# Kernel optimization log

Measured on AMD Instinct MI355X. Metric: run time of the kernel, lower is better.

## Reference

```python
import jax, jax.numpy as jnp
import numpy as np

EPS = 1e-5
NEG = 0.1  # LeakyReLU slope


def _conv(x, w, stride=1, pad=0):
    return jax.lax.conv_general_dilated(
        x, w, (stride, stride), [(pad, pad), (pad, pad)],
        dimension_numbers=('NCHW', 'OIHW', 'NCHW'))


def _bn(x, p):
    # p: [4, C] stacked (gamma, beta, running_mean, running_var); eval-mode BN
    g, b, m, v = p[0], p[1], p[2], p[3]
    inv = g / jnp.sqrt(v + EPS)
    return x * inv[None, :, None, None] + (b - m * inv)[None, :, None, None]


def _lrelu(x):
    return jnp.where(x >= 0, x, NEG * x)


def _mdcn(x, w_off, b_off, w_dcn, b_dcn, G=2, K=3, pad=1):
    # ModulatedDeformConvPack (DCNv2): conv_offset -> (dy, dx, mask), then
    # modulated bilinear sampling + dense contraction with the conv weight.
    B, C, H, W = x.shape
    K2 = K * K
    off = _conv(x, w_off, 1, pad) + b_off[None, :, None, None]  # [B, 3*G*K2, H, W]
    dy, dx, ml = jnp.split(off, 3, axis=1)
    dy = dy.reshape(B, G, K2, H, W)
    dx = dx.reshape(B, G, K2, H, W)
    mask = jax.nn.sigmoid(ml).reshape(B, G, K2, H, W)
    kyv, kxv = np.meshgrid(np.arange(K), np.arange(K), indexing='ij')
    ky = jnp.asarray(kyv.reshape(K2), x.dtype)
    kx = jnp.asarray(kxv.reshape(K2), x.dtype)
    ii = jnp.arange(H, dtype=x.dtype)
    jj = jnp.arange(W, dtype=x.dtype)
    # sample coords: p0 + p_k + offset (stride 1, dilation 1)
    py = ii[None, None, None, :, None] - pad + ky[None, None, :, None, None] + dy
    px = jj[None, None, None, None, :] - pad + kx[None, None, :, None, None] + dx
    Cg = C // G
    # [B, G, H*W, Cg] layout so the bilinear gather indexes a small int tensor
    imgs = x.reshape(B, G, Cg, H, W).transpose(0, 1, 3, 4, 2).reshape(B, G, H * W, Cg)
    y0 = jnp.floor(py)
    x0 = jnp.floor(px)
    N = K2 * H * W
    wy = (py - y0).reshape(B, G, N, 1)
    wx = (px - x0).reshape(B, G, N, 1)

    def gather(yi, xi):
        valid = (yi >= 0) & (yi <= H - 1) & (xi >= 0) & (xi <= W - 1)
        yc = jnp.clip(yi, 0, H - 1).astype(jnp.int32)
        xc = jnp.clip(xi, 0, W - 1).astype(jnp.int32)
        idx = (yc * W + xc).reshape(B, G, N, 1)
        v = jnp.take_along_axis(imgs, idx, axis=2)  # [B, G, N, Cg]
        return v * valid.reshape(B, G, N, 1).astype(x.dtype)

    v00 = gather(y0, x0)
    v01 = gather(y0, x0 + 1)
    v10 = gather(y0 + 1, x0)
    v11 = gather(y0 + 1, x0 + 1)
    val = (v00 * (1 - wy) * (1 - wx) + v01 * (1 - wy) * wx
           + v10 * wy * (1 - wx) + v11 * wy * wx)
    val = (val * mask.reshape(B, G, N, 1)).reshape(B, G, K2, H, W, Cg)
    wr = w_dcn.reshape(w_dcn.shape[0], G, Cg, K2)
    out = jnp.einsum('bgkijc,ogck->boij', val, wr)
    return out + b_dcn[None, :, None, None]


def _forward(x, w_r1, bn_r1, w_r2, bn_r2, w_rs, bn_rs, w_off, b_off,
             w_dcn, b_dcn, bn1, w_c2, bn2, w_ds, bn_ds):
    # ResBlock(in=64, out=128, stride=2): conv3x3/s2-BN-LReLU-conv3x3-BN + 1x1/s2 shortcut
    h = _lrelu(_bn(_conv(x, w_r1, 2, 1), bn_r1))
    h = _bn(_conv(h, w_r2, 1, 1), bn_r2)
    sc = _bn(_conv(x, w_rs, 2, 0), bn_rs)
    h = _lrelu(h + sc)
    # modulated deformable conv 3x3, deformable_groups=2
    h = _lrelu(_bn(_mdcn(h, w_off, b_off, w_dcn, b_dcn), bn1))
    h = _lrelu(_bn(_conv(h, w_c2, 1, 0), bn2))
    # DeconBlock residual (downsample since in!=out, stride!=1)
    res = _bn(_conv(x, w_ds, 2, 0), bn_ds)
    return res + h


def setup_inputs() -> dict:
    key = jax.random.key(0)
    ks = jax.random.split(key, 16)
    f32 = jnp.float32

    def n(k, shape, s):
        return jax.random.normal(k, shape, f32) * s

    def bnp(k, c):
        # gamma, beta, mean, var — var kept >= 0.1 for stability
        return jax.random.uniform(k, (4, c), f32, 0.1, 1.0)

    return {
        'x': n(ks[0], (4, 64, 192, 192), 1.0),
        'w_r1': n(ks[1], (128, 64, 3, 3), 0.04),
        'bn_r1': bnp(ks[2], 128),
        'w_r2': n(ks[3], (128, 128, 3, 3), 0.03),
        'bn_r2': bnp(ks[4], 128),
        'w_rs': n(ks[5], (128, 64, 1, 1), 0.12),
        'bn_rs': bnp(ks[6], 128),
        'w_off': n(ks[7], (54, 128, 3, 3), 0.01),  # small => offsets of a few px
        'b_off': n(ks[8], (54,), 0.1),
        'w_dcn': n(ks[9], (128, 128, 3, 3), 0.03),
        'b_dcn': n(ks[10], (128,), 0.1),
        'bn1': bnp(ks[11], 128),
        'w_c2': n(ks[12], (128, 128, 1, 1), 0.09),
        'bn2': bnp(ks[13], 128),
        'w_ds': n(ks[14], (128, 64, 1, 1), 0.12),
        'bn_ds': bnp(ks[15], 128),
    }


def reference(x, w_r1, bn_r1, w_r2, bn_r2, w_rs, bn_rs, w_off, b_off,
              w_dcn, b_dcn, bn1, w_c2, bn2, w_ds, bn_ds):
    return _forward(x, w_r1, bn_r1, w_r2, bn_r2, w_rs, bn_rs, w_off, b_off,
                    w_dcn, b_dcn, bn1, w_c2, bn2, w_ds, bn_ds)
```

## Files before the change

### kernel.cpp

```cpp
#include <hip/hip_runtime.h>
#include <hip/hip_bf16.h>
#include <cstdint>

#define EPS 1e-5f
#define NEG 0.1f

using bfrag = __attribute__((ext_vector_type(8))) short;
using f32x4 = __attribute__((ext_vector_type(4))) float;
typedef unsigned short ushort_t;

constexpr int B_  = 4,  CIN = 64, H0 = 192, W0 = 192;
constexpr int C_  = 128, H_ = 96, W_ = 96;
constexpr int HW_ = H_ * W_;
constexpr int HW0 = H0 * W0;
constexpr int XS  = 194;
constexpr int TS  = 98;
constexpr int VROW = 392;

__device__ __forceinline__ ushort_t f2bf(float f) {
  unsigned u = __builtin_bit_cast(unsigned, f);
  u += 0x7fffu + ((u >> 16) & 1u);
  return (ushort_t)(u >> 16);
}
__device__ __forceinline__ float loF(unsigned d) {
  return __builtin_bit_cast(float, d << 16);
}
__device__ __forceinline__ float hiF(unsigned d) {
  return __builtin_bit_cast(float, d & 0xFFFF0000u);
}
__device__ __forceinline__ bfrag loadB(const ushort_t* p) {
  return *(const bfrag*)p;
}

#define MFMA4(A0, A1, B0, B1, ACC)                                             \
  ACC[0][0] = __builtin_amdgcn_mfma_f32_16x16x32_bf16(A0, B0, ACC[0][0], 0, 0, 0); \
  ACC[0][1] = __builtin_amdgcn_mfma_f32_16x16x32_bf16(A0, B1, ACC[0][1], 0, 0, 0); \
  ACC[1][0] = __builtin_amdgcn_mfma_f32_16x16x32_bf16(A1, B0, ACC[1][0], 0, 0, 0); \
  ACC[1][1] = __builtin_amdgcn_mfma_f32_16x16x32_bf16(A1, B1, ACC[1][1], 0, 0, 0);

__global__ __launch_bounds__(256)
void k_prep(const float* __restrict__ x,
            const float* __restrict__ w_r1, const float* __restrict__ w_r2,
            const float* __restrict__ w_off, const float* __restrict__ w_dcn,
            const float* __restrict__ w_rs, const float* __restrict__ w_c2,
            const float* __restrict__ w_ds,
            ushort_t* __restrict__ wp_r1, ushort_t* __restrict__ wp_r2,
            ushort_t* __restrict__ wp_off, ushort_t* __restrict__ wp_dcn,
            ushort_t* __restrict__ wp_rs, ushort_t* __restrict__ wp_c2,
            ushort_t* __restrict__ wp_ds,
            ushort_t* __restrict__ xclp, ushort_t* __restrict__ t1p,
            ushort_t* __restrict__ t3p) {
  __shared__ float tile[64][65];
  int bi = blockIdx.x;
  int tid = (int)threadIdx.x;
  auto pack3w = [&](const float* w, ushort_t* wp, int O, int C, int Opad, int b0) {
    int idx = (bi - b0) * 256 + tid;
    int e = idx & 7;
    int lane = (idx >> 3) & 63;
    int fb = idx >> 9;
    int OBQ = Opad / 16;
    int obq = fb % OBQ, s = fb / OBQ;
    int lr = lane & 15, lq = lane >> 4;
    int o = obq * 16 + lr;
    int cq = s % (C / 32), tap = s / (C / 32);
    int c = cq * 32 + lq * 8 + e;
    wp[idx] = (o < O) ? f2bf(w[((size_t)o * C + c) * 9 + tap]) : (ushort_t)0;
  };
  auto pack1w = [&](const float* w, ushort_t* wp, int O, int C, int Opad, int b0) {
    int idx = (bi - b0) * 256 + tid;
    int e = idx & 7;
    int lane = (idx >> 3) & 63;
    int fb = idx >> 9;
    int OBQ = Opad / 16;
    int obq = fb % OBQ, s = fb / OBQ;
    int lr = lane & 15, lq = lane >> 4;
    int o = obq * 16 + lr;
    int c = s * 32 + lq * 8 + e;
    wp[idx] = (o < O) ? f2bf(w[(size_t)o * C + c]) : (ushort_t)0;
  };
  auto border = [&](ushort_t* buf, int N, int C, int b0) {
    int idx = (bi - b0) * 256 + tid;
    int per = 4 * N - 4;
    if (idx >= per * 4) return;
    int b = idx / per, e = idx - b * per;
    int r, s;
    if (e < N) { r = 0; s = e; }
    else if (e < 2 * N) { r = N - 1; s = e - N; }
    else if (e < 3 * N - 2) { r = e - 2 * N + 1; s = 0; }
    else { r = e - (3 * N - 2) + 1; s = N - 1; }
    uint4* p = (uint4*)(buf + ((size_t)(b * N + r) * N + s) * C);
#pragma unroll
    for (int t = 0; t < 16; ++t) { if (t < C / 8) p[t] = make_uint4(0, 0, 0, 0); }
  };
  if      (bi <  288) pack3w(w_r1,  wp_r1, 128,  64, 128, 0);
  else if (bi <  864) pack3w(w_r2,  wp_r2, 128, 128, 128, 288);
  else if (bi < 1152) pack3w(w_off, wp_off, 54, 128,  64, 864);
  else if (bi < 1728) pack3w(w_dcn, wp_dcn, 128, 128, 128, 1152);
  else if (bi < 1760) pack1w(w_rs,  wp_rs, 128,  64, 128, 1728);
  else if (bi < 1824) pack1w(w_c2,  wp_c2, 128, 128, 128, 1760);
  else if (bi < 1856) pack1w(w_ds,  wp_ds, 128,  64, 128, 1824);
  else if (bi < 1869) border(xclp, XS, 64, 1856);
  else if (bi < 1876) border(t1p, TS, 128, 1869);
  else if (bi < 1883) border(t3p, TS, 128, 1876);
  else {
    int bx = bi - 1883;
    int cx = bx % 3;
    int rem = bx / 3;
    int y = rem % 192, b = rem / 192;
    int tx = tid & 63, ty = tid >> 6;
    const float* src = x + (size_t)b * CIN * HW0 + (size_t)y * W0 + cx * 64;
#pragma unroll
    for (int r = 0; r < 16; ++r) {
      int ch = r * 4 + ty;
      tile[ch][tx] = src[(size_t)ch * HW0 + tx];
    }
    __syncthreads();
    ushort_t* dst = xclp + ((size_t)(b * XS + y + 1) * XS + cx * 64 + 1) * 64;
#pragma unroll
    for (int r = 0; r < 16; ++r) {
      int pp = r * 4 + ty;
      dst[(size_t)pp * 64 + tx] = f2bf(tile[tx][pp]);
    }
  }
}

__global__ __launch_bounds__(256)
void k_conv1(const ushort_t* __restrict__ xclp, const ushort_t* __restrict__ wp,
             const float* __restrict__ bnp, ushort_t* __restrict__ t1p) {
  __shared__ ushort_t at[5 * 66 * 64];
  int tid = threadIdx.x, lane = tid & 63, wv = tid >> 6;
  int lr = lane & 15, lq = lane >> 4, ob = wv * 32;
  int j0 = blockIdx.x * 32, i0 = blockIdx.y * 2, b = blockIdx.z;
  for (int t = tid; t < 2640; t += 256) {
    int ky = t / 528, r = t - ky * 528;
    int p = r >> 3, c8 = r & 7;
    const char* src = (const char*)(xclp +
        ((size_t)(b * XS + 2 * i0 + ky) * XS + 2 * j0) * 64) + p * 128 + c8 * 16;
    int db = ((ky * 66 + p) * 128 + c8 * 16) ^ (((p >> 1) & 7) << 4);
    *(uint4*)((char*)at + db) = *(const uint4*)src;
  }
  __syncthreads();
  f32x4 acc[2][2][2] = {};
#pragma unroll
  for (int tap = 0; tap < 9; ++tap) {
    int ky = tap / 3, kx = tap - 3 * ky;
    int pxa = 2 * lr + kx, pxb = 2 * (16 + lr) + kx;
#pragma unroll
    for (int cq = 0; cq < 2; ++cq) {
      int s = tap * 2 + cq;
      bfrag b0 = loadB(wp + (size_t)(s * 8 + wv * 2) * 512 + lane * 8);
      bfrag b1 = loadB(wp + (size_t)(s * 8 + wv * 2 + 1) * 512 + lane * 8);
#pragma unroll
      for (int r = 0; r < 2; ++r) {
        int kr = 2 * r + ky;
        bfrag a0 = *(const bfrag*)((const char*)at +
            (((kr * 66 + pxa) * 128 + cq * 64 + lq * 16) ^ (((pxa >> 1) & 7) << 4)));
        bfrag a1 = *(const bfrag*)((const char*)at +
            (((kr * 66 + pxb) * 128 + cq * 64 + lq * 16) ^ (((pxb >> 1) & 7) << 4)));
        MFMA4(a0, a1, b0, b1, acc[r]);
      }
    }
  }
#pragma unroll
  for (int r = 0; r < 2; ++r) {
    ushort_t* dst = t1p + ((size_t)(b * TS + i0 + r + 1) * TS + j0 + 1) * 128;
#pragma unroll
    for (int nf = 0; nf < 2; ++nf) {
      int o = ob + nf * 16 + lr;
      float inv = bnp[o] * rsqrtf(bnp[384 + o] + EPS);
      float bb = bnp[128 + o] - bnp[256 + o] * inv;
#pragma unroll
      for (int mf = 0; mf < 2; ++mf)
#pragma unroll
        for (int jj = 0; jj < 4; ++jj) {
          int pix = mf * 16 + 4 * lq + jj;
          float v = acc[r][mf][nf][jj] * inv + bb;
          v = v >= 0.f ? v : NEG * v;
          dst[(size_t)pix * 128 + o] = f2bf(v);
        }
    }
  }
}

__global__ __launch_bounds__(256)
void k_conv2(const ushort_t* __restrict__ t1p, const ushort_t* __restrict__ xclp,
             const ushort_t* __restrict__ wp2, const ushort_t* __restrict__ wprs,
             const float* __restrict__ bn2p, const float* __restrict__ bnsp,
             ushort_t* __restrict__ t3p) {
  __shared__ ushort_t at[4 * 34 * 128];
  int tid = threadIdx.x, lane = tid & 63, wv = tid >> 6;
  int lr = lane & 15, lq = lane >> 4, ob = wv * 32;
  int j0 = blockIdx.x * 32, i0 = blockIdx.y * 2, b = blockIdx.z;
  for (int t = tid; t < 2176; t += 256) {
    int ky = t / 544, r = t - ky * 544;
    int p = r >> 4, c16 = r & 15;
    const char* src = (const char*)(t1p +
        ((size_t)(b * TS + i0 + ky) * TS + j0) * 128) + p * 256 + c16 * 16;
    int db = ((ky * 34 + p) * 256 + c16 * 16) ^ ((p & 7) << 4);
    *(uint4*)((char*)at + db) = *(const uint4*)src;
  }
  __syncthreads();
  f32x4 acc[2][2][2] = {};
  f32x4 acs[2][2][2] = {};
#pragma unroll
  for (int tap = 0; tap < 9; ++tap) {
    int ky = tap / 3, kx = tap - 3 * ky;
    int pxa = lr + kx, pxb = 16 + lr + kx;
#pragma unroll
    for (int cq = 0; cq < 4; ++cq) {
      int s = tap * 4 + cq;
      bfrag b0 = loadB(wp2 + (size_t)(s * 8 + wv * 2) * 512 + lane * 8);
      bfrag b1 = loadB(wp2 + (size_t)(s * 8 + wv * 2 + 1) * 512 + lane * 8);
#pragma unroll
      for (int r = 0; r < 2; ++r) {
        int kr = r + ky;
        bfrag a0 = *(const bfrag*)((const char*)at +
            (((kr * 34 + pxa) * 256 + cq * 64 + lq * 16) ^ ((pxa & 7) << 4)));
        bfrag a1 = *(const bfrag*)((const char*)at +
            (((kr * 34 + pxb) * 256 + cq * 64 + lq * 16) ^ ((pxb & 7) << 4)));
        MFMA4(a0, a1, b0, b1, acc[r]);
      }
    }
  }
#pragma unroll
  for (int r = 0; r < 2; ++r) {
    const ushort_t* rowp = xclp + (size_t)(b * XS + 2 * (i0 + r) + 1) * XS * 64;
    const ushort_t* pa = rowp + (size_t)(2 * (j0 + lr) + 1) * 64 + 8 * lq;
    const ushort_t* pb = rowp + (size_t)(2 * (j0 + 16 + lr) + 1) * 64 + 8 * lq;
#pragma unroll
    for (int sq = 0; sq < 2; ++sq) {
      bfrag a0 = loadB(pa + sq * 32);
      bfrag a1 = loadB(pb + sq * 32);
      bfrag b0 = loadB(wprs + (size_t)(sq * 8 + wv * 2) * 512 + lane * 8);
      bfrag b1 = loadB(wprs + (size_t)(sq * 8 + wv * 2 + 1) * 512 + lane * 8);
      MFMA4(a0, a1, b0, b1, acs[r]);
    }
  }
#pragma unroll
  for (int r = 0; r < 2; ++r) {
    ushort_t* dst = t3p + ((size_t)(b * TS + i0 + r + 1) * TS + j0 + 1) * 128;
#pragma unroll
    for (int nf = 0; nf < 2; ++nf) {
      int o = ob + nf * 16 + lr;
      float i2 = bn2p[o] * rsqrtf(bn2p[384 + o] + EPS);
      float b2 = bn2p[128 + o] - bn2p[256 + o] * i2;
      float is = bnsp[o] * rsqrtf(bnsp[384 + o] + EPS);
      float bs = bnsp[128 + o] - bnsp[256 + o] * is;
#pragma unroll
      for (int mf = 0; mf < 2; ++mf)
#pragma unroll
        for (int jj = 0; jj < 4; ++jj) {
          int pix = mf * 16 + 4 * lq + jj;
          float h = acc[r][mf][nf][jj] * i2 + b2 + acs[r][mf][nf][jj] * is + bs;
          h = h >= 0.f ? h : NEG * h;
          dst[(size_t)pix * 128 + o] = f2bf(h);
        }
    }
  }
}

__global__ __launch_bounds__(512)
void k_dcn(const ushort_t* __restrict__ t3p, const ushort_t* __restrict__ wpo,
           const float* __restrict__ boff, const ushort_t* __restrict__ wp,
           const float* __restrict__ bdcn, const float* __restrict__ bnp,
           ushort_t* __restrict__ t4cl) {
  __shared__ char smem[26112];
  __shared__ float offb_lds[32 * 64];
  int tid = threadIdx.x;
  int j0 = blockIdx.x * 32, i = blockIdx.y, b = blockIdx.z;
  int lane = tid & 63, wv = tid >> 6;
  int lr = lane & 15, lq = lane >> 4;

  {
    for (int t = tid; t < 1632; t += 512) {
      int ky = t / 544, r = t - ky * 544;
      int p = r >> 4, c16b = r & 15;
      const char* src = (const char*)(t3p +
          ((size_t)(b * TS + i + ky) * TS + j0 + p) * 128) + c16b * 16;
      int db = ((ky * 34 + p) * 256 + c16b * 16) ^ ((p & 7) << 4);
      *(uint4*)(smem + db) = *(const uint4*)src;
    }
    __syncthreads();
    int ot = wv >> 1, half = wv & 1;
    f32x4 pacc = {};
#pragma unroll
    for (int s = 0; s < 36; ++s) {
      int tap = s >> 2, cq = s & 3;
      int ky = tap / 3, kx = tap - 3 * ky;
      int px = half * 16 + lr + kx;
      bfrag a0 = *(const bfrag*)(smem +
          (((ky * 34 + px) * 256 + cq * 64 + lq * 16) ^ ((px & 7) << 4)));
      bfrag b0 = loadB(wpo + (size_t)(s * 4 + ot) * 512 + lane * 8);
      pacc = __builtin_amdgcn_mfma_f32_16x16x32_bf16(a0, b0, pacc, 0, 0, 0);
    }
    int o = ot * 16 + lr;
    float bias = (o < 54) ? boff[o] : 0.f;
#pragma unroll
    for (int jj = 0; jj < 4; ++jj) {
      int px = half * 16 + 4 * lq + jj;
      offb_lds[px * 64 + o] = pacc[jj] + bias;
    }
    __syncthreads();
  }

  int gq = tid >> 4;
  int c16 = tid & 15;
  int gl = (gq & 3) * 16;
  int my_b0 = 0, my_b1 = 0;
  unsigned my_w00 = 0, my_w10 = 0, my_w01 = 0, my_w11 = 0;
  if (c16 < 9) {
    int k = c16;
    int ky = k / 3, kx = k - 3 * ky;
    int j = j0 + gq;
    const float* ob_ = offb_lds + gq * 64;
#pragma unroll
    for (int g = 0; g < 2; ++g) {
      int gk = g * 9 + k;
      float dy = ob_[gk];
      float dx = ob_[18 + gk];
      float ml = ob_[36 + gk];
      float mk = 1.f / (1.f + __expf(-ml));
      float py = (float)(i - 1 + ky) + dy;
      float px = (float)(j - 1 + kx) + dx;
      float fy = floorf(py), fx = floorf(px);
      float wy = py - fy, wx = px - fx;
      int y0 = (int)fy, x0 = (int)fx;
      bool yv0 = (unsigned)y0 < 96u, yv1 = (unsigned)(y0 + 1) < 96u;
      bool xv0 = (unsigned)x0 < 96u, xv1 = (unsigned)(x0 + 1) < 96u;
      float w00 = (yv0 && xv0) ? (1.f - wy) * (1.f - wx) * mk : 0.f;
      float w01 = (yv0 && xv1) ? (1.f - wy) * wx * mk : 0.f;
      float w10 = (yv1 && xv0) ? wy * (1.f - wx) * mk : 0.f;
      float w11 = (yv1 && xv1) ? wy * wx * mk : 0.f;
      int yb = min(max(y0, -1), 95), xb = min(max(x0, -1), 95);
      int bb = (((yb + 1) * TS + xb + 1) * 128 + g * 64) * 2;
      unsigned pw0 = (unsigned)f2bf(w00) | ((unsigned)f2bf(w01) << 16);
      unsigned pw1 = (unsigned)f2bf(w10) | ((unsigned)f2bf(w11) << 16);
      if (g == 0) { my_b0 = bb; my_w00 = pw0; my_w10 = pw1; }
      else        { my_b1 = bb; my_w01 = pw0; my_w11 = pw1; }
    }
  }
  __syncthreads();

  ushort_t* val = (ushort_t*)smem;
  const char* imgb = (const char*)(t3p + (size_t)b * TS * TS * 128) + c16 * 8;
  char* vrow = (char*)val + gq * (VROW * 2) + c16 * 8;
  int ob = wv * 16;
  f32x4 acc0 = {}, acc1 = {};
#pragma unroll
  for (int c = 0; c < 3; ++c) {
#pragma unroll
    for (int g = 0; g < 2; ++g) {
#pragma unroll
      for (int kc = 0; kc < 3; ++kc) {
        int k = 3 * c + kc;
        int gb = __shfl(g == 0 ? my_b0 : my_b1, gl + k, 64);
        unsigned w0 = (unsigned)__shfl((int)(g == 0 ? my_w00 : my_w01), gl + k, 64);
        unsigned w1 = (unsigned)__shfl((int)(g == 0 ? my_w10 : my_w11), gl + k, 64);
        const char* pA = imgb + gb;
        uint2 d00 = *(const uint2*)pA;
        uint2 d01 = *(const uint2*)(pA + 256);
        uint2 d10 = *(const uint2*)(pA + TS * 256);
        uint2 d11 = *(const uint2*)(pA + TS * 256 + 256);
        float w00 = loF(w0), w01 = hiF(w0);
        float w10 = loF(w1), w11 = hiF(w1);
        unsigned o2[2];
#pragma unroll
        for (int t = 0; t < 2; ++t) {
          unsigned e00 = ((const unsigned*)&d00)[t];
          unsigned e01 = ((const unsigned*)&d01)[t];
          unsigned e10 = ((const unsigned*)&d10)[t];
          unsigned e11 = ((const unsigned*)&d11)[t];
          float slo = loF(e00) * w00 + loF(e01) * w01 + loF(e10) * w10 + loF(e11) * w11;
          float shi = hiF(e00) * w00 + hiF(e01) * w01 + hiF(e10) * w10 + hiF(e11) * w11;
          unsigned u0 = __builtin_bit_cast(unsigned, slo) + 0x8000u;
          unsigned u1 = __builtin_bit_cast(unsigned, shi) + 0x8000u;
          o2[t] = __builtin_amdgcn_perm(u1, u0, 0x07060302u);
        }
        *(uint2*)(vrow + kc * 256 + g * 128) = make_uint2(o2[0], o2[1]);
      }
    }
    __syncthreads();
#pragma unroll
    for (int sl = 0; sl < 12; ++sl) {
      int s = c * 12 + sl;
      bfrag a0 = *(const bfrag*)&val[lr * VROW + 32 * sl + 8 * lq];
      bfrag a1 = *(const bfrag*)&val[(16 + lr) * VROW + 32 * sl + 8 * lq];
      bfrag b0 = loadB(wp + (size_t)(s * 8 + wv) * 512 + lane * 8);
      acc0 = __builtin_amdgcn_mfma_f32_16x16x32_bf16(a0, b0, acc0, 0, 0, 0);
      acc1 = __builtin_amdgcn_mfma_f32_16x16x32_bf16(a1, b0, acc1, 0, 0, 0);
    }
    if (c < 2) __syncthreads();
  }

  {
    ushort_t* dst = t4cl + ((size_t)(b * 96 + i) * 96 + j0) * 128;
    int o = ob + lr;
    float inv = bnp[o] * rsqrtf(bnp[384 + o] + EPS);
    float bb = bnp[128 + o] - bnp[256 + o] * inv;
    float bd = bdcn[o];
#pragma unroll
    for (int jj = 0; jj < 4; ++jj) {
      int p0 = 4 * lq + jj;
      float r0 = (acc0[jj] + bd) * inv + bb;
      r0 = r0 >= 0.f ? r0 : NEG * r0;
      dst[(size_t)p0 * 128 + o] = f2bf(r0);
      float r1 = (acc1[jj] + bd) * inv + bb;
      r1 = r1 >= 0.f ? r1 : NEG * r1;
      dst[(size_t)(16 + p0) * 128 + o] = f2bf(r1);
    }
  }
}

__global__ __launch_bounds__(256)
void k_final(const ushort_t* __restrict__ t4cl, const ushort_t* __restrict__ xclp,
             const ushort_t* __restrict__ wpc2, const ushort_t* __restrict__ wpds,
             const float* __restrict__ bn2p, const float* __restrict__ bndsp,
             float* __restrict__ outp) {
  __shared__ float ol[128 * 36];
  int tid = threadIdx.x, lane = tid & 63, wv = tid >> 6;
  int lr = lane & 15, lq = lane >> 4, ob = wv * 32;
  int j0 = blockIdx.x * 32, i = blockIdx.y, b = blockIdx.z;
  f32x4 acc[2][2] = {};
  f32x4 acs[2][2] = {};
  {
    const ushort_t* rowp = t4cl + ((size_t)(b * 96 + i) * 96 + j0) * 128;
#pragma unroll
    for (int s = 0; s < 4; ++s) {
      bfrag a0 = loadB(rowp + (size_t)lr * 128 + s * 32 + 8 * lq);
      bfrag a1 = loadB(rowp + (size_t)(16 + lr) * 128 + s * 32 + 8 * lq);
      bfrag b0 = loadB(wpc2 + (size_t)(s * 8 + wv * 2) * 512 + lane * 8);
      bfrag b1 = loadB(wpc2 + (size_t)(s * 8 + wv * 2 + 1) * 512 + lane * 8);
      MFMA4(a0, a1, b0, b1, acc);
    }
  }
  {
    const ushort_t* rowx = xclp + (size_t)(b * XS + 2 * i + 1) * XS * 64;
    const ushort_t* pa = rowx + (size_t)(2 * (j0 + lr) + 1) * 64 + 8 * lq;
    const ushort_t* pb = rowx + (size_t)(2 * (j0 + 16 + lr) + 1) * 64 + 8 * lq;
#pragma unroll
    for (int s = 0; s < 2; ++s) {
      bfrag a0 = loadB(pa + s * 32);
      bfrag a1 = loadB(pb + s * 32);
      bfrag b0 = loadB(wpds + (size_t)(s * 8 + wv * 2) * 512 + lane * 8);
      bfrag b1 = loadB(wpds + (size_t)(s * 8 + wv * 2 + 1) * 512 + lane * 8);
      MFMA4(a0, a1, b0, b1, acs);
    }
  }
#pragma unroll
  for (int nf = 0; nf < 2; ++nf) {
    int o = ob + nf * 16 + lr;
    float i2 = bn2p[o] * rsqrtf(bn2p[384 + o] + EPS);
    float b2 = bn2p[128 + o] - bn2p[256 + o] * i2;
    float id = bndsp[o] * rsqrtf(bndsp[384 + o] + EPS);
    float bd = bndsp[128 + o] - bndsp[256 + o] * id;
#pragma unroll
    for (int mf = 0; mf < 2; ++mf)
#pragma unroll
      for (int jj = 0; jj < 4; ++jj) {
        int pix = mf * 16 + 4 * lq + jj;
        float h = acc[mf][nf][jj] * i2 + b2;
        h = h >= 0.f ? h : NEG * h;
        float res = acs[mf][nf][jj] * id + bd;
        ol[o * 36 + pix] = res + h;
      }
  }
  __syncthreads();
#pragma unroll
  for (int r = 0; r < 4; ++r) {
    int idx = r * 256 + tid;
    int o = idx >> 3, p4 = idx & 7;
    f32x4 v = *(const f32x4*)&ol[o * 36 + p4 * 4];
    *(f32x4*)&outp[((size_t)(b * C_ + o) * H_ + i) * W_ + j0 + p4 * 4] = v;
  }
}

extern "C" void kernel_launch(void* const* d_in, const int* in_sizes, int n_in,
                              void* d_out, int out_size, void* d_ws, size_t ws_size,
                              hipStream_t stream) {
  const float* x     = (const float*)d_in[0];
  const float* w_r1  = (const float*)d_in[1];
  const float* bn_r1 = (const float*)d_in[2];
  const float* w_r2  = (const float*)d_in[3];
  const float* bn_r2 = (const float*)d_in[4];
  const float* w_rs  = (const float*)d_in[5];
  const float* bn_rs = (const float*)d_in[6];
  const float* w_off = (const float*)d_in[7];
  const float* b_off = (const float*)d_in[8];
  const float* w_dcn = (const float*)d_in[9];
  const float* b_dcn = (const float*)d_in[10];
  const float* bn1   = (const float*)d_in[11];
  const float* w_c2  = (const float*)d_in[12];
  const float* bn2   = (const float*)d_in[13];
  const float* w_ds  = (const float*)d_in[14];
  const float* bn_ds = (const float*)d_in[15];
  float* out = (float*)d_out;

  ushort_t* base  = (ushort_t*)d_ws;
  ushort_t* xclp  = base;
  ushort_t* t1p   = base + 9634816;
  ushort_t* t3p   = base + 14552064;
  ushort_t* wp_r1 = base + 19469312;
  ushort_t* wp_r2 = wp_r1 + 73728;
  ushort_t* wp_off= wp_r2 + 147456;
  ushort_t* wp_dcn= wp_off + 73728;
  ushort_t* wp_rs = wp_dcn + 147456;
  ushort_t* wp_c2 = wp_rs + 8192;
  ushort_t* wp_ds = wp_c2 + 16384;
  ushort_t* t4cl  = t1p;

  k_prep<<<4187, 256, 0, stream>>>(x, w_r1, w_r2, w_off, w_dcn, w_rs, w_c2,
                                   w_ds, wp_r1, wp_r2, wp_off, wp_dcn, wp_rs,
                                   wp_c2, wp_ds, xclp, t1p, t3p);

  k_conv1<<<dim3(3, 48, 4), 256, 0, stream>>>(xclp, wp_r1, bn_r1, t1p);
  k_conv2<<<dim3(3, 48, 4), 256, 0, stream>>>(t1p, xclp, wp_r2, wp_rs, bn_r2, bn_rs, t3p);
  k_dcn  <<<dim3(3, 96, 4), 512, 0, stream>>>(t3p, wp_off, b_off, wp_dcn, b_dcn, bn1, t4cl);
  k_final<<<dim3(3, 96, 4), 256, 0, stream>>>(t4cl, xclp, wp_c2, wp_ds, bn2, bn_ds, out);
}
```

Before: 121.7 us.

## Fuse final 1x1 conv, downsample shortcut and residual add into DCN kernel

Folds the k_final kernel into k_dcn. The BN+LeakyReLU output of the deformable conv now goes to shared memory with a padded stride of 136 instead of being written to global memory. The same block then runs the 1x1 conv2 and the downsample shortcut with MFMA and writes the fp32 output. This removes one launch and a global write and read of the intermediate t4 tensor. In exchange it adds shared-memory reuse and an extra barrier in an already heavy kernel, and each wave now covers only 16 output channels.

```diff
diff --git a/kernel.cpp b/kernel.cpp
--- a/kernel.cpp
+++ b/kernel.cpp
@@ -263,9 +263,11 @@
 void k_dcn(const ushort_t* __restrict__ t3p, const ushort_t* __restrict__ wpo,
            const float* __restrict__ boff, const ushort_t* __restrict__ wp,
            const float* __restrict__ bdcn, const float* __restrict__ bnp,
-           ushort_t* __restrict__ t4cl) {
+           const ushort_t* __restrict__ xclp, const ushort_t* __restrict__ wpc2,
+           const ushort_t* __restrict__ wpds, const float* __restrict__ bn2p,
+           const float* __restrict__ bndsp, float* __restrict__ outp) {
   __shared__ char smem[26112];
-  __shared__ float offb_lds[32 * 64];
+  __shared__ float aux_f[2304];
   int tid = threadIdx.x;
   int j0 = blockIdx.x * 32, i = blockIdx.y, b = blockIdx.z;
   int lane = tid & 63, wv = tid >> 6;
@@ -298,7 +300,7 @@
 #pragma unroll
     for (int jj = 0; jj < 4; ++jj) {
       int px = half * 16 + 4 * lq + jj;
-      offb_lds[px * 64 + o] = pacc[jj] + bias;
+      aux_f[px * 64 + o] = pacc[jj] + bias;
     }
     __syncthreads();
   }
@@ -312,7 +314,7 @@
     int k = c16;
     int ky = k / 3, kx = k - 3 * ky;
     int j = j0 + gq;
-    const float* ob_ = offb_lds + gq * 64;
+    const float* ob_ = aux_f + gq * 64;
 #pragma unroll
     for (int g = 0; g < 2; ++g) {
       int gk = g * 9 + k;
@@ -392,8 +394,8 @@
     if (c < 2) __syncthreads();
   }
 
+  ushort_t* t4t = (ushort_t*)aux_f;
   {
-    ushort_t* dst = t4cl + ((size_t)(b * 96 + i) * 96 + j0) * 128;
     int o = ob + lr;
     float inv = bnp[o] * rsqrtf(bnp[384 + o] + EPS);
     float bb = bnp[128 + o] - bnp[256 + o] * inv;
@@ -403,35 +405,22 @@
       int p0 = 4 * lq + jj;
       float r0 = (acc0[jj] + bd) * inv + bb;
       r0 = r0 >= 0.f ? r0 : NEG * r0;
-      dst[(size_t)p0 * 128 + o] = f2bf(r0);
+      t4t[p0 * 136 + o] = f2bf(r0);
       float r1 = (acc1[jj] + bd) * inv + bb;
       r1 = r1 >= 0.f ? r1 : NEG * r1;
-      dst[(size_t)(16 + p0) * 128 + o] = f2bf(r1);
-    }
-  }
-}
-
-__global__ __launch_bounds__(256)
-void k_final(const ushort_t* __restrict__ t4cl, const ushort_t* __restrict__ xclp,
-             const ushort_t* __restrict__ wpc2, const ushort_t* __restrict__ wpds,
-             const float* __restrict__ bn2p, const float* __restrict__ bndsp,
-             float* __restrict__ outp) {
-  __shared__ float ol[128 * 36];
-  int tid = threadIdx.x, lane = tid & 63, wv = tid >> 6;
-  int lr = lane & 15, lq = lane >> 4, ob = wv * 32;
-  int j0 = blockIdx.x * 32, i = blockIdx.y, b = blockIdx.z;
-  f32x4 acc[2][2] = {};
-  f32x4 acs[2][2] = {};
-  {
-    const ushort_t* rowp = t4cl + ((size_t)(b * 96 + i) * 96 + j0) * 128;
-#pragma unroll
-    for (int s = 0; s < 4; ++s) {
-      bfrag a0 = loadB(rowp + (size_t)lr * 128 + s * 32 + 8 * lq);
-      bfrag a1 = loadB(rowp + (size_t)(16 + lr) * 128 + s * 32 + 8 * lq);
-      bfrag b0 = loadB(wpc2 + (size_t)(s * 8 + wv * 2) * 512 + lane * 8);
-      bfrag b1 = loadB(wpc2 + (size_t)(s * 8 + wv * 2 + 1) * 512 + lane * 8);
-      MFMA4(a0, a1, b0, b1, acc);
-    }
+      t4t[(16 + p0) * 136 + o] = f2bf(r1);
+    }
+  }
+  __syncthreads();
+
+  f32x4 f0 = {}, f1 = {}, s0 = {}, s1 = {};
+#pragma unroll
+  for (int s = 0; s < 4; ++s) {
+    bfrag a0 = *(const bfrag*)&t4t[lr * 136 + s * 32 + 8 * lq];
+    bfrag a1 = *(const bfrag*)&t4t[(16 + lr) * 136 + s * 32 + 8 * lq];
+    bfrag b0 = loadB(wpc2 + (size_t)(s * 8 + wv) * 512 + lane * 8);
+    f0 = __builtin_amdgcn_mfma_f32_16x16x32_bf16(a0, b0, f0, 0, 0, 0);
+    f1 = __builtin_amdgcn_mfma_f32_16x16x32_bf16(a1, b0, f1, 0, 0, 0);
   }
   {
     const ushort_t* rowx = xclp + (size_t)(b * XS + 2 * i + 1) * XS * 64;
@@ -441,33 +430,33 @@
     for (int s = 0; s < 2; ++s) {
       bfrag a0 = loadB(pa + s * 32);
       bfrag a1 = loadB(pb + s * 32);
-      bfrag b0 = loadB(wpds + (size_t)(s * 8 + wv * 2) * 512 + lane * 8);
-      bfrag b1 = loadB(wpds + (size_t)(s * 8 + wv * 2 + 1) * 512 + lane * 8);
-      MFMA4(a0, a1, b0, b1, acs);
-    }
-  }
-#pragma unroll
-  for (int nf = 0; nf < 2; ++nf) {
-    int o = ob + nf * 16 + lr;
+      bfrag b0 = loadB(wpds + (size_t)(s * 8 + wv) * 512 + lane * 8);
+      s0 = __builtin_amdgcn_mfma_f32_16x16x32_bf16(a0, b0, s0, 0, 0, 0);
+      s1 = __builtin_amdgcn_mfma_f32_16x16x32_bf16(a1, b0, s1, 0, 0, 0);
+    }
+  }
+  float* ol = (float*)smem;
+  {
+    int o = ob + lr;
     float i2 = bn2p[o] * rsqrtf(bn2p[384 + o] + EPS);
     float b2 = bn2p[128 + o] - bn2p[256 + o] * i2;
     float id = bndsp[o] * rsqrtf(bndsp[384 + o] + EPS);
-    float bd = bndsp[128 + o] - bndsp[256 + o] * id;
-#pragma unroll
-    for (int mf = 0; mf < 2; ++mf)
-#pragma unroll
-      for (int jj = 0; jj < 4; ++jj) {
-        int pix = mf * 16 + 4 * lq + jj;
-        float h = acc[mf][nf][jj] * i2 + b2;
-        h = h >= 0.f ? h : NEG * h;
-        float res = acs[mf][nf][jj] * id + bd;
-        ol[o * 36 + pix] = res + h;
-      }
+    float bd2 = bndsp[128 + o] - bndsp[256 + o] * id;
+#pragma unroll
+    for (int jj = 0; jj < 4; ++jj) {
+      int p0 = 4 * lq + jj;
+      float h0 = f0[jj] * i2 + b2;
+      h0 = h0 >= 0.f ? h0 : NEG * h0;
+      ol[o * 36 + p0] = s0[jj] * id + bd2 + h0;
+      float h1 = f1[jj] * i2 + b2;
+      h1 = h1 >= 0.f ? h1 : NEG * h1;
+      ol[o * 36 + 16 + p0] = s1[jj] * id + bd2 + h1;
+    }
   }
   __syncthreads();
 #pragma unroll
-  for (int r = 0; r < 4; ++r) {
-    int idx = r * 256 + tid;
+  for (int r = 0; r < 2; ++r) {
+    int idx = r * 512 + tid;
     int o = idx >> 3, p4 = idx & 7;
     f32x4 v = *(const f32x4*)&ol[o * 36 + p4 * 4];
     *(f32x4*)&outp[((size_t)(b * C_ + o) * H_ + i) * W_ + j0 + p4 * 4] = v;
@@ -506,7 +495,6 @@
   ushort_t* wp_rs = wp_dcn + 147456;
   ushort_t* wp_c2 = wp_rs + 8192;
   ushort_t* wp_ds = wp_c2 + 16384;
-  ushort_t* t4cl  = t1p;
 
   k_prep<<<4187, 256, 0, stream>>>(x, w_r1, w_r2, w_off, w_dcn, w_rs, w_c2,
                                    w_ds, wp_r1, wp_r2, wp_off, wp_dcn, wp_rs,
@@ -514,6 +502,6 @@
 
   k_conv1<<<dim3(3, 48, 4), 256, 0, stream>>>(xclp, wp_r1, bn_r1, t1p);
   k_conv2<<<dim3(3, 48, 4), 256, 0, stream>>>(t1p, xclp, wp_r2, wp_rs, bn_r2, bn_rs, t3p);
-  k_dcn  <<<dim3(3, 96, 4), 512, 0, stream>>>(t3p, wp_off, b_off, wp_dcn, b_dcn, bn1, t4cl);
-  k_final<<<dim3(3, 96, 4), 256, 0, stream>>>(t4cl, xclp, wp_c2, wp_ds, bn2, bn_ds, out);
-}
+  k_dcn  <<<dim3(3, 96, 4), 512, 0, stream>>>(t3p, wp_off, b_off, wp_dcn, b_dcn, bn1,
+                                              xclp, wp_c2, wp_ds, bn2, bn_ds, out);
+}
```

New measurement: 115.9 us. -4.8%, faster.
